# Performance work log

Hardware: AMD Instinct MI355X
Metric: run time of the kernel (lower is better)

The kernel has to match this reference:

```python
import jax, jax.numpy as jnp
import numpy as np

N_HEADS = 16
ROPE_BASE = 10000.0


def _apply_rope(t, cos, sin):
    # t: (B, H, S, D); cos/sin: (S, D/2). Rotate-half convention.
    d2 = t.shape[-1] // 2
    t1, t2 = t[..., :d2], t[..., d2:]
    return jnp.concatenate([t1 * cos - t2 * sin, t2 * cos + t1 * sin], axis=-1)


def setup_inputs() -> dict:
    key = jax.random.key(0)
    k0, k1, k2, k3, k4 = jax.random.split(key, 5)
    B, S, E = 4, 2048, 1024
    scale = 0.02
    x = jax.random.normal(k0, (B, S, E), dtype=jnp.float32)
    w_qkv = jax.random.normal(k1, (E, 3 * E), dtype=jnp.float32) * scale
    b_qkv = jnp.zeros((3 * E,), dtype=jnp.float32)
    w_proj = jax.random.normal(k2, (E, E), dtype=jnp.float32) * scale
    b_proj = jnp.zeros((E,), dtype=jnp.float32)
    return {"x": x, "w_qkv": w_qkv, "b_qkv": b_qkv, "w_proj": w_proj, "b_proj": b_proj}


def reference(x, w_qkv, b_qkv, w_proj, b_proj):
    B, S, E = x.shape
    H = N_HEADS
    D = E // H
    # fused QKV projection
    qkv = x @ w_qkv + b_qkv                      # (B, S, 3E)
    q, k, v = jnp.split(qkv, 3, axis=-1)
    def to_heads(t):
        return t.reshape(B, S, H, D).transpose(0, 2, 1, 3)  # (B, H, S, D)
    q, k, v = to_heads(q), to_heads(k), to_heads(v)
    # RoPE (rotate-half)
    inv_freq = ROPE_BASE ** (-jnp.arange(0, D, 2, dtype=jnp.float32) / D)  # (D/2,)
    pos = jnp.arange(S, dtype=jnp.float32)
    freqs = pos[:, None] * inv_freq[None, :]     # (S, D/2)
    cos, sin = jnp.cos(freqs), jnp.sin(freqs)
    q = _apply_rope(q, cos, sin)
    k = _apply_rope(k, cos, sin)
    # causal SDPA
    scores = jnp.einsum('bhqd,bhkd->bhqk', q, k) / jnp.sqrt(jnp.float32(D))
    causal = jnp.tril(jnp.ones((S, S), dtype=bool))
    scores = jnp.where(causal, scores, jnp.float32(-1e30))
    probs = jax.nn.softmax(scores, axis=-1)
    out = jnp.einsum('bhqk,bhkd->bhqd', probs, v)  # (B, H, S, D)
    out = out.transpose(0, 2, 1, 3).reshape(B, S, E)
    # output projection (dropout is identity at p=0 / eval)
    return out @ w_proj + b_proj
```

## Files before the change

kernel.cpp:

```cpp
#include <hip/hip_runtime.h>

typedef unsigned short u16;
typedef __bf16 bf16x8 __attribute__((ext_vector_type(8)));
typedef float f32x4 __attribute__((ext_vector_type(4)));

__device__ __forceinline__ u16 f2b(float f) {
    unsigned u = __builtin_bit_cast(unsigned, f);
    unsigned r = (u + 0x7fffu + ((u >> 16) & 1u)) >> 16;
    return (u16)r;
}
#if __has_builtin(__builtin_amdgcn_cvt_pk_bf16_f32)
typedef __bf16 bf16x2_t __attribute__((ext_vector_type(2)));
__device__ __forceinline__ unsigned pk2(float a, float b) {
    return __builtin_bit_cast(unsigned, __builtin_amdgcn_cvt_pk_bf16_f32(a, b));
}
#else
__device__ __forceinline__ unsigned pk2(float a, float b) {
    return (unsigned)f2b(a) | ((unsigned)f2b(b) << 16);
}
#endif
#if __has_builtin(__builtin_amdgcn_exp2f)
#define EXP2F(x) __builtin_amdgcn_exp2f(x)
#else
#define EXP2F(x) exp2f(x)
#endif

__device__ __forceinline__ void gl_lds16(const u16* g, u16* l) {
    __builtin_amdgcn_global_load_lds(
        (const __attribute__((address_space(1))) unsigned*)(const void*)g,
        (__attribute__((address_space(3))) unsigned*)(void*)l, 16, 0, 0);
}

__global__ __launch_bounds__(256) void k_rope_table(float2* __restrict__ tab) {
    int i = blockIdx.x * 256 + threadIdx.x;
    int s = i >> 5, d = i & 31;
    const float C0 = 0.4152410118609203f;
    float inv_freq = exp2f(-C0 * (float)d);
    float sn, cs;
    sincosf((float)s * inv_freq, &sn, &cs);
    tab[i] = make_float2(cs, sn);
}

__global__ __launch_bounds__(256) void k_convert(const float* __restrict__ in,
                                                 u16* __restrict__ out, int n8) {
    int i = blockIdx.x * 256 + threadIdx.x;
    if (i >= n8) return;
    const float4* p = (const float4*)(in + (size_t)i * 8);
    float4 a = p[0], b = p[1];
    u16 t[8] = {f2b(a.x), f2b(a.y), f2b(a.z), f2b(a.w),
                f2b(b.x), f2b(b.y), f2b(b.z), f2b(b.w)};
    *(uint4*)(out + (size_t)i * 8) = *(const uint4*)t;
}

__global__ __launch_bounds__(256) void k_transpose_bf16(const float* __restrict__ in,
                                                        u16* __restrict__ out,
                                                        int R, int C) {
    __shared__ u16 tile[64][72];
    int tc = blockIdx.x * 64;
    int tr = blockIdx.y * 64;
    for (int i = threadIdx.x; i < 4096; i += 256) {
        int r = i >> 6, c = i & 63;
        tile[c][r] = f2b(in[(size_t)(tr + r) * C + tc + c]);
    }
    __syncthreads();
    for (int i = threadIdx.x; i < 4096; i += 256) {
        int r = i >> 6, c = i & 63;
        out[(size_t)(tc + r) * R + tr + c] = tile[r][c];
    }
}

__device__ __forceinline__ void gemm_mainloop(const u16* __restrict__ Ab,
                                              const u16* __restrict__ Bb, int K,
                                              u16* As, u16* Bs, int tid,
                                              f32x4 (&acc)[4][4]) {
    const int wave = tid >> 6, lane = tid & 63;
    const int col = lane & 15, quad = lane >> 4;
    const int wm = wave >> 1, wn = wave & 1;
    const int lrow = lane >> 2, lk = (lane & 3) * 8;
    u16* ldsA0 = As + (wave * 16) * 32;
    u16* ldsA1 = As + (64 + wave * 16) * 32;
    u16* ldsB0 = Bs + (wave * 16) * 32;
    u16* ldsB1 = Bs + (64 + wave * 16) * 32;
    const u16* gA0 = Ab + (size_t)(wave * 16 + lrow) * K + lk;
    const u16* gA1 = gA0 + (size_t)64 * K;
    const u16* gB0 = Bb + (size_t)(wave * 16 + lrow) * K + lk;
    const u16* gB1 = gB0 + (size_t)64 * K;
    for (int k0 = 0; k0 < K; k0 += 64) {
        if (k0) __syncthreads();
#pragma unroll
        for (int kh = 0; kh < 2; ++kh) {
            int ko = k0 + kh * 32;
            gl_lds16(gA0 + ko, ldsA0 + kh * 4096);
            gl_lds16(gA1 + ko, ldsA1 + kh * 4096);
            gl_lds16(gB0 + ko, ldsB0 + kh * 4096);
            gl_lds16(gB1 + ko, ldsB1 + kh * 4096);
        }
        __syncthreads();
#pragma unroll
        for (int kh = 0; kh < 2; ++kh) {
            bf16x8 af[4], bfr[4];
#pragma unroll
            for (int mt = 0; mt < 4; ++mt)
                af[mt] = *(const bf16x8*)(As + kh * 4096 +
                                          (wm * 64 + mt * 16 + col) * 32 + quad * 8);
#pragma unroll
            for (int nt = 0; nt < 4; ++nt)
                bfr[nt] = *(const bf16x8*)(Bs + kh * 4096 +
                                           (wn * 64 + nt * 16 + col) * 32 + quad * 8);
#pragma unroll
            for (int mt = 0; mt < 4; ++mt)
#pragma unroll
                for (int nt = 0; nt < 4; ++nt)
                    acc[mt][nt] = __builtin_amdgcn_mfma_f32_16x16x32_bf16(
                        af[mt], bfr[nt], acc[mt][nt], 0, 0, 0);
        }
    }
}

__global__ __launch_bounds__(256) void k_gemm_qkv_rope(
    const u16* __restrict__ A, const u16* __restrict__ Bt,
    const float* __restrict__ bias, const float2* __restrict__ tab,
    u16* __restrict__ Qr, u16* __restrict__ Kr, u16* __restrict__ Vt) {
    __shared__ __align__(16) u16 smem[16384];
    u16* As = smem;
    u16* Bs = smem + 8192;
    const int K = 1024;
    int tid = threadIdx.x;
    int lane = tid & 63, wave = tid >> 6;
    int col = lane & 15, quad = lane >> 4;
    int wm = wave >> 1, wn = wave & 1;
    int mBase = blockIdx.y * 128;
    int nBase = blockIdx.x * 128;
    f32x4 acc[4][4] = {};
    gemm_mainloop(A + (size_t)mBase * K, Bt + (size_t)nBase * K, K, As, Bs, tid, acc);

    int region = nBase >> 10;
    int n64 = nBase + wn * 64;
    int h = (n64 & 1023) >> 6;
    if (region < 2) {
        __syncthreads();
        float qs = (region == 0) ? 0.18033688011112042f : 1.0f;
#pragma unroll
        for (int nt = 0; nt < 2; ++nt) {
            int d1 = nt * 16 + col;
            float b1 = bias[n64 + d1];
            float b2 = bias[n64 + d1 + 32];
            int nl = wn * 64 + nt * 16 + col;
#pragma unroll
            for (int mt = 0; mt < 4; ++mt) {
                int mlb = wm * 64 + mt * 16 + quad * 4;
#pragma unroll
                for (int r = 0; r < 4; ++r) {
                    int mloc = mlb + r;
                    int s = (mBase + mloc) & 2047;
                    float2 t = tab[s * 32 + d1];
                    float t1 = acc[mt][nt][r] + b1;
                    float t2 = acc[mt][nt + 2][r] + b2;
                    int sw = (mloc & 7) << 3;
                    smem[mloc * 128 + (nl ^ sw)] = f2b((t1 * t.x - t2 * t.y) * qs);
                    smem[mloc * 128 + ((nl + 32) ^ sw)] = f2b((t2 * t.x + t1 * t.y) * qs);
                }
            }
        }
        __syncthreads();
        u16* outp = (region == 0) ? Qr : Kr;
#pragma unroll
        for (int p = 0; p < 8; ++p) {
            int lin = p * 256 + tid;
            int mloc = lin >> 4;
            int c8 = (lin & 15) << 3;
            uint4 v = *(const uint4*)(smem + mloc * 128 + (c8 ^ ((mloc & 7) << 3)));
            int m = mBase + mloc;
            int s = m & 2047, b = m >> 11;
            int ng = (nBase & 1023) + c8;
            *(uint4*)(Qr == outp || Kr == outp
                          ? outp + ((size_t)((b * 16 + (ng >> 6)) * 2048 + s)) * 64 +
                                (ng & 63)
                          : outp) = v;
        }
    } else {
        int b = mBase >> 11;
        int sb0 = mBase & 2047;
#pragma unroll
        for (int nt = 0; nt < 4; ++nt) {
            int d = nt * 16 + col;
            float bv = bias[n64 + d];
            u16* vrow = Vt + ((size_t)((b * 16 + h) * 64 + d)) * 2048;
#pragma unroll
            for (int mt = 0; mt < 4; ++mt) {
                int s = sb0 + wm * 64 + mt * 16 + quad * 4;
                uint2 w;
                w.x = pk2(acc[mt][nt][0] + bv, acc[mt][nt][1] + bv);
                w.y = pk2(acc[mt][nt][2] + bv, acc[mt][nt][3] + bv);
                *(uint2*)(vrow + s) = w;
            }
        }
    }
}

__global__ __launch_bounds__(256, 4) void k_attn(const u16* __restrict__ Qr,
                                                 const u16* __restrict__ Kr,
                                                 const u16* __restrict__ Vt,
                                                 u16* __restrict__ O) {
    __shared__ __align__(16) u16 Ks[2][64 * 72];
    __shared__ __align__(16) u16 Vs[2][64 * 72];
    int tid = threadIdx.x, wave = tid >> 6, lane = tid & 63;
    int col = lane & 15, quad = lane >> 4;
    int id = blockIdx.x + (blockIdx.y << 4);
    int xcd = id & 7, seq = id >> 3;
    int head = xcd * 8 + (seq >> 4);
    int qb = 15 - (seq & 15);
    int b = head >> 4, h = head & 15;
    size_t headQ = (size_t)head * 2048 * 64;
    size_t headV = (size_t)head * 64 * 2048;
    int r0 = tid >> 3, kc = tid & 7;
    int rb72 = ((col >> 2) * 8 + (col & 3)) * 72;

    int t0 = 2 * qb, t1 = t0 + 1;
    int myq0 = qb * 128 + wave * 16 + col;
    int myq1 = myq0 + 64;
    const u16* qp0 = Qr + headQ + (size_t)myq0 * 64;
    const u16* qp1 = Qr + headQ + (size_t)myq1 * 64;
    bf16x8 aq00 = *(const bf16x8*)(qp0 + quad * 8);
    bf16x8 aq01 = *(const bf16x8*)(qp0 + 32 + quad * 8);
    bf16x8 aq10 = *(const bf16x8*)(qp1 + quad * 8);
    bf16x8 aq11 = *(const bf16x8*)(qp1 + 32 + quad * 8);
    f32x4 o0[4] = {}, o1[4] = {};
    float l0 = 0.f, l1 = 0.f;

    const u16* kg = Kr + headQ + (size_t)r0 * 64 + kc * 8;
    const u16* vg = Vt + headV + (size_t)r0 * 2048 + kc * 8;
    {
        uint4 kr0 = *(const uint4*)kg;
        uint4 kr1 = *(const uint4*)(kg + 32 * 64);
        uint4 vr0 = *(const uint4*)vg;
        uint4 vr1 = *(const uint4*)(vg + 32 * 2048);
        *(uint4*)(Ks[0] + r0 * 72 + kc * 8) = kr0;
        *(uint4*)(Ks[0] + (r0 + 32) * 72 + kc * 8) = kr1;
        *(uint4*)(Vs[0] + r0 * 72 + kc * 8) = vr0;
        *(uint4*)(Vs[0] + (r0 + 32) * 72 + kc * 8) = vr1;
    }
    __syncthreads();

    for (int j = 0; j <= t1; ++j) {
        int cur = j & 1;
        uint4 kr0, kr1, vr0, vr1;
        if (j < t1) {
            const u16* kgn = kg + (size_t)(j + 1) * 64 * 64;
            const u16* vgn = vg + (j + 1) * 64;
            kr0 = *(const uint4*)kgn;
            kr1 = *(const uint4*)(kgn + 32 * 64);
            vr0 = *(const uint4*)vgn;
            vr1 = *(const uint4*)(vgn + 32 * 2048);
        }
        bool d0 = (j <= t0);
        const u16* KsC = Ks[cur];
        const u16* VsC = Vs[cur];
        f32x4 s0[4], s1[4];
#pragma unroll
        for (int nt = 0; nt < 4; ++nt) {
            const u16* kp = KsC + rb72 + ((nt & 1) * 32 + (nt >> 1) * 4) * 72;
            bf16x8 ak0 = *(const bf16x8*)(kp + quad * 8);
            bf16x8 ak1 = *(const bf16x8*)(kp + 32 + quad * 8);
            if (d0) {
                f32x4 z = {};
                z = __builtin_amdgcn_mfma_f32_16x16x32_bf16(ak0, aq00, z, 0, 0, 0);
                s0[nt] = __builtin_amdgcn_mfma_f32_16x16x32_bf16(ak1, aq01, z, 0, 0, 0);
            }
            f32x4 z = {};
            z = __builtin_amdgcn_mfma_f32_16x16x32_bf16(ak0, aq10, z, 0, 0, 0);
            s1[nt] = __builtin_amdgcn_mfma_f32_16x16x32_bf16(ak1, aq11, z, 0, 0, 0);
        }
        if (j == t0) {
#pragma unroll
            for (int nt = 0; nt < 4; ++nt) {
                int keyb = j * 64 + (nt & 1) * 32 + quad * 8 + (nt >> 1) * 4;
#pragma unroll
                for (int r = 0; r < 4; ++r)
                    if (keyb + r > myq0) s0[nt][r] = -3.0e38f;
            }
        }
        if (j == t1) {
#pragma unroll
            for (int nt = 0; nt < 4; ++nt) {
                int keyb = j * 64 + (nt & 1) * 32 + quad * 8 + (nt >> 1) * 4;
#pragma unroll
                for (int r = 0; r < 4; ++r)
                    if (keyb + r > myq1) s1[nt][r] = -3.0e38f;
            }
        }
        unsigned P40[8], P41[8];
        if (d0) {
#pragma unroll
            for (int nt = 0; nt < 4; ++nt) {
                float p0 = EXP2F(s0[nt][0]);
                float p1 = EXP2F(s0[nt][1]);
                float p2 = EXP2F(s0[nt][2]);
                float p3 = EXP2F(s0[nt][3]);
                l0 += (p0 + p1) + (p2 + p3);
                P40[2 * nt] = pk2(p0, p1);
                P40[2 * nt + 1] = pk2(p2, p3);
            }
        }
#pragma unroll
        for (int nt = 0; nt < 4; ++nt) {
            float p0 = EXP2F(s1[nt][0]);
            float p1 = EXP2F(s1[nt][1]);
            float p2 = EXP2F(s1[nt][2]);
            float p3 = EXP2F(s1[nt][3]);
            l1 += (p0 + p1) + (p2 + p3);
            P41[2 * nt] = pk2(p0, p1);
            P41[2 * nt + 1] = pk2(p2, p3);
        }
#pragma unroll
        for (int kk = 0; kk < 2; ++kk) {
            uint4 bw0, bw1;
            bw0.x = P40[2 * kk];
            bw0.y = P40[2 * kk + 1];
            bw0.z = P40[2 * kk + 4];
            bw0.w = P40[2 * kk + 5];
            bw1.x = P41[2 * kk];
            bw1.y = P41[2 * kk + 1];
            bw1.z = P41[2 * kk + 4];
            bw1.w = P41[2 * kk + 5];
            bf16x8 bp0 = __builtin_bit_cast(bf16x8, bw0);
            bf16x8 bp1 = __builtin_bit_cast(bf16x8, bw1);
#pragma unroll
            for (int mt = 0; mt < 4; ++mt) {
                bf16x8 av = *(const bf16x8*)(VsC + (mt * 16 + col) * 72 + kk * 32 + quad * 8);
                if (d0)
                    o0[mt] = __builtin_amdgcn_mfma_f32_16x16x32_bf16(av, bp0, o0[mt], 0, 0, 0);
                o1[mt] = __builtin_amdgcn_mfma_f32_16x16x32_bf16(av, bp1, o1[mt], 0, 0, 0);
            }
        }
        if (j < t1) {
            int nxt = cur ^ 1;
            *(uint4*)(Ks[nxt] + r0 * 72 + kc * 8) = kr0;
            *(uint4*)(Ks[nxt] + (r0 + 32) * 72 + kc * 8) = kr1;
            *(uint4*)(Vs[nxt] + r0 * 72 + kc * 8) = vr0;
            *(uint4*)(Vs[nxt] + (r0 + 32) * 72 + kc * 8) = vr1;
            __syncthreads();
        }
    }
    l0 += __shfl_xor(l0, 16);
    l0 += __shfl_xor(l0, 32);
    l1 += __shfl_xor(l1, 16);
    l1 += __shfl_xor(l1, 32);
    float inv0 = 1.0f / l0, inv1 = 1.0f / l1;
    u16* orow0 = O + (size_t)(b * 2048 + myq0) * 1024 + h * 64;
    u16* orow1 = O + (size_t)(b * 2048 + myq1) * 1024 + h * 64;
#pragma unroll
    for (int mt = 0; mt < 4; ++mt) {
        uint2 w0, w1;
        w0.x = pk2(o0[mt][0] * inv0, o0[mt][1] * inv0);
        w0.y = pk2(o0[mt][2] * inv0, o0[mt][3] * inv0);
        w1.x = pk2(o1[mt][0] * inv1, o1[mt][1] * inv1);
        w1.y = pk2(o1[mt][2] * inv1, o1[mt][3] * inv1);
        *(uint2*)(orow0 + mt * 16 + quad * 4) = w0;
        *(uint2*)(orow1 + mt * 16 + quad * 4) = w1;
    }
}

__global__ __launch_bounds__(256) void k_gemm_proj(const u16* __restrict__ A,
                                                   const u16* __restrict__ Bt,
                                                   const float* __restrict__ bias,
                                                   float* __restrict__ out) {
    __shared__ __align__(16) u16 As[2 * 128 * 32];
    __shared__ __align__(16) u16 Bs[2 * 128 * 32];
    const int K = 1024;
    int tid = threadIdx.x;
    int lane = tid & 63, wave = tid >> 6;
    int col = lane & 15, quad = lane >> 4;
    int wm = wave >> 1, wn = wave & 1;
    int mBase = blockIdx.y * 128;
    int nBase = blockIdx.x * 128;
    f32x4 acc[4][4] = {};
    gemm_mainloop(A + (size_t)mBase * K, Bt + (size_t)nBase * K, K, As, Bs, tid, acc);
#pragma unroll
    for (int nt = 0; nt < 4; ++nt) {
        int n = nBase + wn * 64 + nt * 16 + col;
        float bv = bias[n];
#pragma unroll
        for (int mt = 0; mt < 4; ++mt) {
            int m = mBase + wm * 64 + mt * 16 + quad * 4;
#pragma unroll
            for (int r = 0; r < 4; ++r)
                out[(size_t)(m + r) * 1024 + n] = acc[mt][nt][r] + bv;
        }
    }
}

extern "C" void kernel_launch(void* const* d_in, const int* in_sizes, int n_in,
                              void* d_out, int out_size, void* d_ws, size_t ws_size,
                              hipStream_t stream) {
    const float* x = (const float*)d_in[0];
    const float* w_qkv = (const float*)d_in[1];
    const float* b_qkv = (const float*)d_in[2];
    const float* w_proj = (const float*)d_in[3];
    const float* b_proj = (const float*)d_in[4];
    float* out = (float*)d_out;
    char* ws = (char*)d_ws;
    u16* x_bf = (u16*)(ws);
    u16* wqkvT = (u16*)(ws + 16777216);
    u16* wprojT = (u16*)(ws + 23068672);
    u16* Qr = (u16*)(ws + 25165824);
    u16* Kr = (u16*)(ws + 41943040);
    u16* Vt = (u16*)(ws + 58720256);
    u16* AO = (u16*)(ws + 75497472);
    float2* tab = (float2*)(ws + 75497472);

    k_rope_table<<<256, 256, 0, stream>>>(tab);
    k_convert<<<4096, 256, 0, stream>>>(x, x_bf, 1048576);
    k_transpose_bf16<<<dim3(48, 16), 256, 0, stream>>>(w_qkv, wqkvT, 1024, 3072);
    k_transpose_bf16<<<dim3(16, 16), 256, 0, stream>>>(w_proj, wprojT, 1024, 1024);
    k_gemm_qkv_rope<<<dim3(24, 64), 256, 0, stream>>>(x_bf, wqkvT, b_qkv, tab, Qr, Kr, Vt);
    k_attn<<<dim3(16, 64), 256, 0, stream>>>(Qr, Kr, Vt, AO);
    k_gemm_proj<<<dim3(8, 64), 256, 0, stream>>>(AO, wprojT, b_proj, out);
}
```

Baseline: 280.4 us.

## Pair short and long causal query tiles per block for balanced attention work

Each attention block now handles two 64-row query tiles in sequence, tile 31-t and then tile t, where it used to handle one 128-row tile. Every block therefore does the same number of KV iterations, which removes the causal load imbalance and the idle sub-tile work. In exchange each wave carries only one Q tile per KV load, so the K/V tiles reused per block are halved, and K/V shared-memory traffic and per-phase syncs go up.

```diff
diff --git a/kernel.cpp b/kernel.cpp
--- a/kernel.cpp
+++ b/kernel.cpp
@@ -207,157 +207,117 @@
     int tid = threadIdx.x, wave = tid >> 6, lane = tid & 63;
     int col = lane & 15, quad = lane >> 4;
     int id = blockIdx.x + (blockIdx.y << 4);
-    int xcd = id & 7, seq = id >> 3;
-    int head = xcd * 8 + (seq >> 4);
-    int qb = 15 - (seq & 15);
+    int xcd = id & 7, w = id >> 3;
+    int head = xcd * 8 + (w & 7);
+    int tsel = w >> 3;
     int b = head >> 4, h = head & 15;
     size_t headQ = (size_t)head * 2048 * 64;
     size_t headV = (size_t)head * 64 * 2048;
     int r0 = tid >> 3, kc = tid & 7;
     int rb72 = ((col >> 2) * 8 + (col & 3)) * 72;
-
-    int t0 = 2 * qb, t1 = t0 + 1;
-    int myq0 = qb * 128 + wave * 16 + col;
-    int myq1 = myq0 + 64;
-    const u16* qp0 = Qr + headQ + (size_t)myq0 * 64;
-    const u16* qp1 = Qr + headQ + (size_t)myq1 * 64;
-    bf16x8 aq00 = *(const bf16x8*)(qp0 + quad * 8);
-    bf16x8 aq01 = *(const bf16x8*)(qp0 + 32 + quad * 8);
-    bf16x8 aq10 = *(const bf16x8*)(qp1 + quad * 8);
-    bf16x8 aq11 = *(const bf16x8*)(qp1 + 32 + quad * 8);
-    f32x4 o0[4] = {}, o1[4] = {};
-    float l0 = 0.f, l1 = 0.f;
-
-    const u16* kg = Kr + headQ + (size_t)r0 * 64 + kc * 8;
-    const u16* vg = Vt + headV + (size_t)r0 * 2048 + kc * 8;
-    {
-        uint4 kr0 = *(const uint4*)kg;
-        uint4 kr1 = *(const uint4*)(kg + 32 * 64);
-        uint4 vr0 = *(const uint4*)vg;
-        uint4 vr1 = *(const uint4*)(vg + 32 * 2048);
-        *(uint4*)(Ks[0] + r0 * 72 + kc * 8) = kr0;
-        *(uint4*)(Ks[0] + (r0 + 32) * 72 + kc * 8) = kr1;
-        *(uint4*)(Vs[0] + r0 * 72 + kc * 8) = vr0;
-        *(uint4*)(Vs[0] + (r0 + 32) * 72 + kc * 8) = vr1;
-    }
-    __syncthreads();
-
-    for (int j = 0; j <= t1; ++j) {
-        int cur = j & 1;
-        uint4 kr0, kr1, vr0, vr1;
-        if (j < t1) {
-            const u16* kgn = kg + (size_t)(j + 1) * 64 * 64;
-            const u16* vgn = vg + (j + 1) * 64;
-            kr0 = *(const uint4*)kgn;
-            kr1 = *(const uint4*)(kgn + 32 * 64);
-            vr0 = *(const uint4*)vgn;
-            vr1 = *(const uint4*)(vgn + 32 * 2048);
-        }
-        bool d0 = (j <= t0);
-        const u16* KsC = Ks[cur];
-        const u16* VsC = Vs[cur];
-        f32x4 s0[4], s1[4];
-#pragma unroll
-        for (int nt = 0; nt < 4; ++nt) {
-            const u16* kp = KsC + rb72 + ((nt & 1) * 32 + (nt >> 1) * 4) * 72;
-            bf16x8 ak0 = *(const bf16x8*)(kp + quad * 8);
-            bf16x8 ak1 = *(const bf16x8*)(kp + 32 + quad * 8);
-            if (d0) {
+    const u16* kg0 = Kr + headQ + (size_t)r0 * 64 + kc * 8;
+    const u16* vg0 = Vt + headV + (size_t)r0 * 2048 + kc * 8;
+
+#pragma unroll 1
+    for (int phase = 0; phase < 2; ++phase) {
+        int T = phase ? tsel : 31 - tsel;
+        int myq = T * 64 + wave * 16 + col;
+        const u16* qp = Qr + headQ + (size_t)myq * 64;
+        bf16x8 aq0 = *(const bf16x8*)(qp + quad * 8);
+        bf16x8 aq1 = *(const bf16x8*)(qp + 32 + quad * 8);
+        f32x4 o[4] = {};
+        float l = 0.f;
+
+        __syncthreads();
+        {
+            uint4 a0 = *(const uint4*)kg0;
+            uint4 a1 = *(const uint4*)(kg0 + 32 * 64);
+            uint4 v0 = *(const uint4*)vg0;
+            uint4 v1 = *(const uint4*)(vg0 + 32 * 2048);
+            *(uint4*)(Ks[0] + r0 * 72 + kc * 8) = a0;
+            *(uint4*)(Ks[0] + (r0 + 32) * 72 + kc * 8) = a1;
+            *(uint4*)(Vs[0] + r0 * 72 + kc * 8) = v0;
+            *(uint4*)(Vs[0] + (r0 + 32) * 72 + kc * 8) = v1;
+        }
+        __syncthreads();
+
+        for (int j = 0; j <= T; ++j) {
+            int cur = j & 1;
+            uint4 kr0, kr1, vr0, vr1;
+            if (j < T) {
+                const u16* kgn = kg0 + (size_t)(j + 1) * 64 * 64;
+                const u16* vgn = vg0 + (j + 1) * 64;
+                kr0 = *(const uint4*)kgn;
+                kr1 = *(const uint4*)(kgn + 32 * 64);
+                vr0 = *(const uint4*)vgn;
+                vr1 = *(const uint4*)(vgn + 32 * 2048);
+            }
+            const u16* KsC = Ks[cur];
+            const u16* VsC = Vs[cur];
+            f32x4 s[4];
+#pragma unroll
+            for (int nt = 0; nt < 4; ++nt) {
+                const u16* kp = KsC + rb72 + ((nt & 1) * 32 + (nt >> 1) * 4) * 72;
+                bf16x8 ak0 = *(const bf16x8*)(kp + quad * 8);
+                bf16x8 ak1 = *(const bf16x8*)(kp + 32 + quad * 8);
                 f32x4 z = {};
-                z = __builtin_amdgcn_mfma_f32_16x16x32_bf16(ak0, aq00, z, 0, 0, 0);
-                s0[nt] = __builtin_amdgcn_mfma_f32_16x16x32_bf16(ak1, aq01, z, 0, 0, 0);
-            }
-            f32x4 z = {};
-            z = __builtin_amdgcn_mfma_f32_16x16x32_bf16(ak0, aq10, z, 0, 0, 0);
-            s1[nt] = __builtin_amdgcn_mfma_f32_16x16x32_bf16(ak1, aq11, z, 0, 0, 0);
-        }
-        if (j == t0) {
+                z = __builtin_amdgcn_mfma_f32_16x16x32_bf16(ak0, aq0, z, 0, 0, 0);
+                s[nt] = __builtin_amdgcn_mfma_f32_16x16x32_bf16(ak1, aq1, z, 0, 0, 0);
+            }
+            if (j == T) {
+#pragma unroll
+                for (int nt = 0; nt < 4; ++nt) {
+                    int keyb = j * 64 + (nt & 1) * 32 + quad * 8 + (nt >> 1) * 4;
+#pragma unroll
+                    for (int r = 0; r < 4; ++r)
+                        if (keyb + r > myq) s[nt][r] = -3.0e38f;
+                }
+            }
+            unsigned P4[8];
 #pragma unroll
             for (int nt = 0; nt < 4; ++nt) {
-                int keyb = j * 64 + (nt & 1) * 32 + quad * 8 + (nt >> 1) * 4;
-#pragma unroll
-                for (int r = 0; r < 4; ++r)
-                    if (keyb + r > myq0) s0[nt][r] = -3.0e38f;
-            }
-        }
-        if (j == t1) {
-#pragma unroll
-            for (int nt = 0; nt < 4; ++nt) {
-                int keyb = j * 64 + (nt & 1) * 32 + quad * 8 + (nt >> 1) * 4;
-#pragma unroll
-                for (int r = 0; r < 4; ++r)
-                    if (keyb + r > myq1) s1[nt][r] = -3.0e38f;
-            }
-        }
-        unsigned P40[8], P41[8];
-        if (d0) {
-#pragma unroll
-            for (int nt = 0; nt < 4; ++nt) {
-                float p0 = EXP2F(s0[nt][0]);
-                float p1 = EXP2F(s0[nt][1]);
-                float p2 = EXP2F(s0[nt][2]);
-                float p3 = EXP2F(s0[nt][3]);
-                l0 += (p0 + p1) + (p2 + p3);
-                P40[2 * nt] = pk2(p0, p1);
-                P40[2 * nt + 1] = pk2(p2, p3);
-            }
-        }
-#pragma unroll
-        for (int nt = 0; nt < 4; ++nt) {
-            float p0 = EXP2F(s1[nt][0]);
-            float p1 = EXP2F(s1[nt][1]);
-            float p2 = EXP2F(s1[nt][2]);
-            float p3 = EXP2F(s1[nt][3]);
-            l1 += (p0 + p1) + (p2 + p3);
-            P41[2 * nt] = pk2(p0, p1);
-            P41[2 * nt + 1] = pk2(p2, p3);
-        }
-#pragma unroll
-        for (int kk = 0; kk < 2; ++kk) {
-            uint4 bw0, bw1;
-            bw0.x = P40[2 * kk];
-            bw0.y = P40[2 * kk + 1];
-            bw0.z = P40[2 * kk + 4];
-            bw0.w = P40[2 * kk + 5];
-            bw1.x = P41[2 * kk];
-            bw1.y = P41[2 * kk + 1];
-            bw1.z = P41[2 * kk + 4];
-            bw1.w = P41[2 * kk + 5];
-            bf16x8 bp0 = __builtin_bit_cast(bf16x8, bw0);
-            bf16x8 bp1 = __builtin_bit_cast(bf16x8, bw1);
-#pragma unroll
-            for (int mt = 0; mt < 4; ++mt) {
-                bf16x8 av = *(const bf16x8*)(VsC + (mt * 16 + col) * 72 + kk * 32 + quad * 8);
-                if (d0)
-                    o0[mt] = __builtin_amdgcn_mfma_f32_16x16x32_bf16(av, bp0, o0[mt], 0, 0, 0);
-                o1[mt] = __builtin_amdgcn_mfma_f32_16x16x32_bf16(av, bp1, o1[mt], 0, 0, 0);
-            }
-        }
-        if (j < t1) {
-            int nxt = cur ^ 1;
-            *(uint4*)(Ks[nxt] + r0 * 72 + kc * 8) = kr0;
-            *(uint4*)(Ks[nxt] + (r0 + 32) * 72 + kc * 8) = kr1;
-            *(uint4*)(Vs[nxt] + r0 * 72 + kc * 8) = vr0;
-            *(uint4*)(Vs[nxt] + (r0 + 32) * 72 + kc * 8) = vr1;
-            __syncthreads();
-        }
-    }
-    l0 += __shfl_xor(l0, 16);
-    l0 += __shfl_xor(l0, 32);
-    l1 += __shfl_xor(l1, 16);
-    l1 += __shfl_xor(l1, 32);
-    float inv0 = 1.0f / l0, inv1 = 1.0f / l1;
-    u16* orow0 = O + (size_t)(b * 2048 + myq0) * 1024 + h * 64;
-    u16* orow1 = O + (size_t)(b * 2048 + myq1) * 1024 + h * 64;
-#pragma unroll
-    for (int mt = 0; mt < 4; ++mt) {
-        uint2 w0, w1;
-        w0.x = pk2(o0[mt][0] * inv0, o0[mt][1] * inv0);
-        w0.y = pk2(o0[mt][2] * inv0, o0[mt][3] * inv0);
-        w1.x = pk2(o1[mt][0] * inv1, o1[mt][1] * inv1);
-        w1.y = pk2(o1[mt][2] * inv1, o1[mt][3] * inv1);
-        *(uint2*)(orow0 + mt * 16 + quad * 4) = w0;
-        *(uint2*)(orow1 + mt * 16 + quad * 4) = w1;
+                float p0 = EXP2F(s[nt][0]);
+                float p1 = EXP2F(s[nt][1]);
+                float p2 = EXP2F(s[nt][2]);
+                float p3 = EXP2F(s[nt][3]);
+                l += (p0 + p1) + (p2 + p3);
+                P4[2 * nt] = pk2(p0, p1);
+                P4[2 * nt + 1] = pk2(p2, p3);
+            }
+#pragma unroll
+            for (int kk = 0; kk < 2; ++kk) {
+                uint4 bw;
+                bw.x = P4[2 * kk];
+                bw.y = P4[2 * kk + 1];
+                bw.z = P4[2 * kk + 4];
+                bw.w = P4[2 * kk + 5];
+                bf16x8 bp = __builtin_bit_cast(bf16x8, bw);
+#pragma unroll
+                for (int mt = 0; mt < 4; ++mt) {
+                    bf16x8 av = *(const bf16x8*)(VsC + (mt * 16 + col) * 72 + kk * 32 + quad * 8);
+                    o[mt] = __builtin_amdgcn_mfma_f32_16x16x32_bf16(av, bp, o[mt], 0, 0, 0);
+                }
+            }
+            if (j < T) {
+                int nxt = cur ^ 1;
+                *(uint4*)(Ks[nxt] + r0 * 72 + kc * 8) = kr0;
+                *(uint4*)(Ks[nxt] + (r0 + 32) * 72 + kc * 8) = kr1;
+                *(uint4*)(Vs[nxt] + r0 * 72 + kc * 8) = vr0;
+                *(uint4*)(Vs[nxt] + (r0 + 32) * 72 + kc * 8) = vr1;
+                __syncthreads();
+            }
+        }
+        l += __shfl_xor(l, 16);
+        l += __shfl_xor(l, 32);
+        float inv = 1.0f / l;
+        u16* orow = O + (size_t)(b * 2048 + myq) * 1024 + h * 64;
+#pragma unroll
+        for (int mt = 0; mt < 4; ++mt) {
+            uint2 w2;
+            w2.x = pk2(o[mt][0] * inv, o[mt][1] * inv);
+            w2.y = pk2(o[mt][2] * inv, o[mt][3] * inv);
+            *(uint2*)(orow + mt * 16 + quad * 4) = w2;
+        }
     }
 }
 
```

After: 256.3 us. 8.6% less time.
